# Kernel optimization log

Hardware: AMD Instinct MI355X
Metric: run time of the kernel (lower is better)

## Reference

```python
import jax, jax.numpy as jnp
import numpy as np

NUM_EXPERTS = 8
TOP_K = 2
HIDDEN = 1024
INTER = 3584
TOKENS = 16384


def setup_inputs() -> dict:
    key = jax.random.key(0)
    k0, k1, k2, k3, k4 = jax.random.split(key, 5)
    s = 0.02
    return {
        "hidden_states": jax.random.normal(k0, (TOKENS, HIDDEN), dtype=jnp.float32),
        "gate_w": jax.random.normal(k1, (NUM_EXPERTS, HIDDEN), dtype=jnp.float32) * s,
        "w1": jax.random.normal(k2, (NUM_EXPERTS, INTER, HIDDEN), dtype=jnp.float32) * s,
        "w3": jax.random.normal(k3, (NUM_EXPERTS, INTER, HIDDEN), dtype=jnp.float32) * s,
        "w2": jax.random.normal(k4, (NUM_EXPERTS, HIDDEN, INTER), dtype=jnp.float32) * s,
    }


def reference(hidden_states, gate_w, w1, w3, w2):
    # Router: logits -> softmax -> top-k -> renormalize (Mixtral gating)
    router_logits = jnp.einsum("th,eh->te", hidden_states, gate_w)  # [T, E]
    probs = jax.nn.softmax(router_logits, axis=-1)
    topk_w, topk_idx = jax.lax.top_k(probs, TOP_K)                  # [T, K]
    topk_w = topk_w / jnp.sum(topk_w, axis=-1, keepdims=True)
    # Dense combine weights: [T, E], zero for unselected experts
    combine = jnp.sum(
        jax.nn.one_hot(topk_idx, NUM_EXPERTS, dtype=hidden_states.dtype)
        * topk_w[..., None],
        axis=1,
    )
    out = jnp.zeros_like(hidden_states)
    for e in range(NUM_EXPERTS):  # small fixed expert loop
        h = jnp.einsum("th,ih->ti", hidden_states, w1[e])   # gate proj
        u = jnp.einsum("th,ih->ti", hidden_states, w3[e])   # up proj
        act = jax.nn.silu(h) * u                             # SwiGLU
        y = jnp.einsum("ti,hi->th", act, w2[e])              # down proj
        out = out + combine[:, e:e + 1] * y
    return out
```

## Files before the change

### kernel.cpp

```cpp
#include <hip/hip_runtime.h>
#include <hip/hip_bf16.h>

#define T_TOKENS 16384
#define HID 1024
#define NEXP 8
#define INTER 3584
#define PAIRS (2*T_TOKENS)
#define PAD_MAX (PAIRS + NEXP*128)

using f32x4    = __attribute__((ext_vector_type(4))) float;
using bfrag    = __attribute__((ext_vector_type(8))) short;
using float4_t = __attribute__((ext_vector_type(4))) float;
using ushort8_t = __attribute__((ext_vector_type(8))) unsigned short;

__device__ inline unsigned short f2bf(float f){
    unsigned u = __float_as_uint(f);
    u += 0x7FFFu + ((u >> 16) & 1u);
    return (unsigned short)(u >> 16);
}

__device__ inline void gload16(const unsigned short* g, unsigned short* l){
    __builtin_amdgcn_global_load_lds(
        (const __attribute__((address_space(1))) void*)g,
        (__attribute__((address_space(3))) void*)l, 16, 0, 0);
}

#define BAR_VM8() asm volatile("s_waitcnt vmcnt(8)\n\ts_barrier" ::: "memory")
#define BAR_VM0() asm volatile("s_waitcnt vmcnt(0)\n\ts_barrier" ::: "memory")
#define BAR_PLAIN() asm volatile("s_barrier" ::: "memory")

__device__ inline int xcd_swz(int flat, int nwg){
    int q = nwg >> 3, r = nwg & 7;
    int xcd = flat & 7, idx = flat >> 3;
    return (xcd < r ? xcd*(q+1) : r*(q+1) + (xcd - r)*q) + idx;
}

__device__ inline void st_decode(int sw, int nM, int nP, int STM,
                                 int& mt, int& p){
    int stSize = STM * nP;
    int st = sw / stSize;
    int rem = sw - st * stSize;
    int base = st * STM;
    int stM = (base + STM <= nM) ? STM : (nM - base);
    p  = rem / stM;
    mt = base + (rem - p * stM);
}

__global__ __launch_bounds__(256) void conv_bf16_kernel(
    const float* __restrict__ in, unsigned short* __restrict__ out, int n)
{
    int i0 = (blockIdx.x * 256 + threadIdx.x) * 8;
    int stride = gridDim.x * 256 * 8;
    for (int i = i0; i < n; i += stride){
        float4_t a = *reinterpret_cast<const float4_t*>(in + i);
        float4_t b = *reinterpret_cast<const float4_t*>(in + i + 4);
        ushort8_t o;
        o[0]=f2bf(a.x); o[1]=f2bf(a.y); o[2]=f2bf(a.z); o[3]=f2bf(a.w);
        o[4]=f2bf(b.x); o[5]=f2bf(b.y); o[6]=f2bf(b.z); o[7]=f2bf(b.w);
        *reinterpret_cast<ushort8_t*>(out + i) = o;
    }
}

__global__ __launch_bounds__(256) void router_kernel(
    const float* __restrict__ x, const float* __restrict__ gw,
    int* __restrict__ topk_idx, float* __restrict__ topk_w)
{
    int wave = threadIdx.x >> 6;
    int lane = threadIdx.x & 63;
    int t = blockIdx.x * 4 + wave;

    float acc[NEXP];
#pragma unroll
    for (int e = 0; e < NEXP; ++e) acc[e] = 0.f;

    const float* xr = x + (size_t)t * HID;
    for (int hb = 0; hb < HID; hb += 64){
        float xv = xr[hb + lane];
#pragma unroll
        for (int e = 0; e < NEXP; ++e)
            acc[e] += xv * gw[e * HID + hb + lane];
    }
#pragma unroll
    for (int e = 0; e < NEXP; ++e){
#pragma unroll
        for (int s = 32; s > 0; s >>= 1)
            acc[e] += __shfl_xor(acc[e], s, 64);
    }
    if (lane == 0){
        int e0 = 0; float m0 = acc[0];
#pragma unroll
        for (int e = 1; e < NEXP; ++e) if (acc[e] > m0){ m0 = acc[e]; e0 = e; }
        int e1 = -1; float m1 = -1e30f;
#pragma unroll
        for (int e = 0; e < NEXP; ++e) if (e != e0 && acc[e] > m1){ m1 = acc[e]; e1 = e; }
        float p1 = __expf(m1 - m0);
        float inv = 1.f / (1.f + p1);
        topk_idx[2*t]   = e0;
        topk_idx[2*t+1] = e1;
        topk_w[2*t]   = inv;
        topk_w[2*t+1] = p1 * inv;
    }
}

__global__ __launch_bounds__(256) void hist_kernel(
    const int* __restrict__ topk_idx, int* __restrict__ counts)
{
    __shared__ int h[NEXP];
    if (threadIdx.x < NEXP) h[threadIdx.x] = 0;
    __syncthreads();
    int i0 = blockIdx.x * 256 + threadIdx.x;
    for (int i = i0; i < PAIRS; i += gridDim.x * 256)
        atomicAdd(&h[topk_idx[i]], 1);
    __syncthreads();
    if (threadIdx.x < NEXP) atomicAdd(&counts[threadIdx.x], h[threadIdx.x]);
}

__global__ void scan_kernel(const int* __restrict__ counts, int* __restrict__ offp)
{
    if (threadIdx.x == 0 && blockIdx.x == 0){
        int s = 0;
        for (int e = 0; e < NEXP; ++e){
            offp[e] = s;
            s += (counts[e] + 127) & ~127;
        }
        offp[NEXP] = s;
    }
}

__global__ __launch_bounds__(128) void padfill_kernel(
    const int* __restrict__ counts, const int* __restrict__ offp,
    int* __restrict__ pair_token, float* __restrict__ pair_w)
{
    int e = blockIdx.x;
    int base = offp[e];
    int aligned = offp[e+1] - base;
    for (int s = counts[e] + threadIdx.x; s < aligned; s += 128){
        pair_token[base + s] = (base + s) & (T_TOKENS - 1);
        pair_w[base + s] = 0.f;
    }
}

__global__ __launch_bounds__(256) void scatter_kernel(
    const int* __restrict__ topk_idx, const float* __restrict__ topk_w,
    const int* __restrict__ offp, int* __restrict__ cursors,
    int* __restrict__ pair_token, float* __restrict__ pair_w)
{
    __shared__ int hist[NEXP], base[NEXP], lcur[NEXP];
    int tid = threadIdx.x;
    if (tid < NEXP){ hist[tid] = 0; lcur[tid] = 0; }
    __syncthreads();

    int t = blockIdx.x * 256 + tid;
    int e0 = topk_idx[2*t], e1 = topk_idx[2*t + 1];
    atomicAdd(&hist[e0], 1);
    atomicAdd(&hist[e1], 1);
    __syncthreads();

    if (tid < NEXP) base[tid] = atomicAdd(&cursors[tid], hist[tid]);
    __syncthreads();

    int r0 = atomicAdd(&lcur[e0], 1);
    int r1 = atomicAdd(&lcur[e1], 1);
    int p0 = offp[e0] + base[e0] + r0;
    int p1 = offp[e1] + base[e1] + r1;
    pair_token[p0] = t;  pair_w[p0] = topk_w[2*t];
    pair_token[p1] = t;  pair_w[p1] = topk_w[2*t + 1];
}

__global__ __launch_bounds__(256) void gemm_act_kernel(
    const unsigned short* __restrict__ xb,
    const unsigned short* __restrict__ w1b,
    const unsigned short* __restrict__ w3b,
    const int* __restrict__ offp,
    const int* __restrict__ pair_token, const float* __restrict__ pair_w,
    unsigned short* __restrict__ act, int r0)
{
    int nP = gridDim.x, nM = gridDim.y;
    int sw = xcd_swz(blockIdx.y * nP + blockIdx.x, nP * nM);
    int mt, p;
    st_decode(sw, nM, nP, 8, mt, p);
    int by = mt, bx = p;

    int R = r0 + by * 128;
    if (R >= offp[NEXP]) return;
    int e = 0;
    while (offp[e+1] <= R) ++e;
    int icol0 = bx * 64;

    __shared__ alignas(16) unsigned short As0[128*64], As1[128*64];
    __shared__ alignas(16) unsigned short B10[64*64],  B11[64*64];
    __shared__ alignas(16) unsigned short B30[64*64],  B31[64*64];
    __shared__ int   toks[128];
    __shared__ float pws[128];

    int tid = threadIdx.x;
    if (tid < 128){
        toks[tid] = pair_token[R + tid];
        pws[tid]  = pair_w[R + tid];
    }
    __syncthreads();

    int w = tid >> 6, lane = tid & 63;
    int wm = w >> 1, wn = w & 1;
    int lr = lane >> 3;
    int l15 = lane & 15;
    int swz8 = ((lane & 7) ^ lr) * 8;

    size_t asrc[4];
#pragma unroll
    for (int i = 0; i < 4; ++i)
        asrc[i] = (size_t)toks[w*32 + i*8 + lr] * HID + swz8;

    const unsigned short* w1e = w1b + (size_t)e * INTER * HID;
    const unsigned short* w3e = w3b + (size_t)e * INTER * HID;
    size_t bsrc[2];
#pragma unroll
    for (int i = 0; i < 2; ++i)
        bsrc[i] = (size_t)(icol0 + w*16 + i*8 + lr) * HID + swz8;

    int ccol[2];
#pragma unroll
    for (int kk = 0; kk < 2; ++kk)
        ccol[kk] = (((kk*4 + (lane >> 4)) ^ (lane & 7)) * 8);

    f32x4 acc_h[4][2], acc_u[4][2];
#pragma unroll
    for (int m = 0; m < 4; ++m)
#pragma unroll
        for (int n = 0; n < 2; ++n){
            acc_h[m][n] = (f32x4){0.f,0.f,0.f,0.f};
            acc_u[m][n] = (f32x4){0.f,0.f,0.f,0.f};
        }

    auto stageT = [&](unsigned short* As, unsigned short* B1s, unsigned short* B3s, int t){
        int k0 = t * 64;
#pragma unroll
        for (int i = 0; i < 4; ++i) gload16(xb  + asrc[i] + k0, As  + (w*32 + i*8)*64);
#pragma unroll
        for (int i = 0; i < 2; ++i) gload16(w1e + bsrc[i] + k0, B1s + (w*16 + i*8)*64);
#pragma unroll
        for (int i = 0; i < 2; ++i) gload16(w3e + bsrc[i] + k0, B3s + (w*16 + i*8)*64);
    };

    auto computeT = [&](const unsigned short* As, const unsigned short* B1s, const unsigned short* B3s){
        __builtin_amdgcn_s_setprio(1);
#pragma unroll
        for (int kk = 0; kk < 2; ++kk){
            int cc = ccol[kk];
            bfrag a[4];
#pragma unroll
            for (int m = 0; m < 4; ++m)
                a[m] = *reinterpret_cast<const bfrag*>(&As[(wm*64 + m*16 + l15)*64 + cc]);
#pragma unroll
            for (int n = 0; n < 2; ++n){
                bfrag b1 = *reinterpret_cast<const bfrag*>(&B1s[(wn*32 + n*16 + l15)*64 + cc]);
                bfrag b3 = *reinterpret_cast<const bfrag*>(&B3s[(wn*32 + n*16 + l15)*64 + cc]);
#pragma unroll
                for (int m = 0; m < 4; ++m){
                    acc_h[m][n] = __builtin_amdgcn_mfma_f32_16x16x32_bf16(a[m], b1, acc_h[m][n], 0, 0, 0);
                    acc_u[m][n] = __builtin_amdgcn_mfma_f32_16x16x32_bf16(a[m], b3, acc_u[m][n], 0, 0, 0);
                }
            }
        }
        __builtin_amdgcn_s_setprio(0);
    };

    const int NT = HID / 64;
    stageT(As0, B10, B30, 0);
    stageT(As1, B11, B31, 1);
#pragma unroll 1
    for (int t = 0; t < NT - 2; t += 2){
        BAR_VM8();
        computeT(As0, B10, B30);
        BAR_PLAIN();
        stageT(As0, B10, B30, t + 2);
        BAR_VM8();
        computeT(As1, B11, B31);
        BAR_PLAIN();
        stageT(As1, B11, B31, t + 3);
    }
    BAR_VM8();
    computeT(As0, B10, B30);
    BAR_VM0();
    computeT(As1, B11, B31);

    size_t arow0 = (size_t)(by * 128) * INTER;
#pragma unroll
    for (int m = 0; m < 4; ++m){
#pragma unroll
        for (int n = 0; n < 2; ++n){
#pragma unroll
            for (int j = 0; j < 4; ++j){
                int rl = wm*64 + m*16 + (lane >> 4)*4 + j;
                float h = acc_h[m][n][j];
                float u = acc_u[m][n][j];
                float v = pws[rl] * h * u / (1.f + __expf(-h));
                int ic = icol0 + wn*32 + n*16 + l15;
                act[arow0 + (size_t)rl * INTER + ic] = f2bf(v);
            }
        }
    }
}

__global__ __launch_bounds__(256) void gemm2_kernel(
    const unsigned short* __restrict__ act,
    const unsigned short* __restrict__ w2b,
    const int* __restrict__ offp,
    const int* __restrict__ pair_token,
    float* __restrict__ out, int r0)
{
    int nP = gridDim.x, nM = gridDim.y;
    int sw = xcd_swz(blockIdx.y * nP + blockIdx.x, nP * nM);
    int mt, p;
    st_decode(sw, nM, nP, 4, mt, p);
    int by = mt, bx = p;

    int R = r0 + by * 128;
    if (R >= offp[NEXP]) return;
    int e = 0;
    while (offp[e+1] <= R) ++e;
    int h0 = bx * 128;

    __shared__ alignas(16) unsigned short As0[128*64], As1[128*64];
    __shared__ alignas(16) unsigned short Bs0[128*64], Bs1[128*64];
    __shared__ int toks[128];

    int tid = threadIdx.x;
    if (tid < 128) toks[tid] = pair_token[R + tid];
    __syncthreads();

    int w = tid >> 6, lane = tid & 63;
    int wm = w >> 1, wn = w & 1;
    int lr = lane >> 3;
    int l15 = lane & 15;
    int swz8 = ((lane & 7) ^ lr) * 8;

    const unsigned short* w2e = w2b + (size_t)e * HID * INTER;
    size_t arow0 = (size_t)(by * 128) * INTER;

    size_t asrc[4], bsrc[4];
#pragma unroll
    for (int i = 0; i < 4; ++i){
        asrc[i] = arow0 + (size_t)(w*32 + i*8 + lr) * INTER + swz8;
        bsrc[i] = (size_t)(h0 + w*32 + i*8 + lr) * INTER + swz8;
    }

    int ccol[2];
#pragma unroll
    for (int kk = 0; kk < 2; ++kk)
        ccol[kk] = (((kk*4 + (lane >> 4)) ^ (lane & 7)) * 8);

    f32x4 acc[4][4];
#pragma unroll
    for (int m = 0; m < 4; ++m)
#pragma unroll
        for (int n = 0; n < 4; ++n)
            acc[m][n] = (f32x4){0.f,0.f,0.f,0.f};

    auto stageT = [&](unsigned short* As, unsigned short* Bs, int t){
        int kc = t * 64;
#pragma unroll
        for (int i = 0; i < 4; ++i) gload16(act + asrc[i] + kc, As + (w*32 + i*8)*64);
#pragma unroll
        for (int i = 0; i < 4; ++i) gload16(w2e + bsrc[i] + kc, Bs + (w*32 + i*8)*64);
    };

    auto computeT = [&](const unsigned short* As, const unsigned short* Bs){
        __builtin_amdgcn_s_setprio(1);
#pragma unroll
        for (int kk = 0; kk < 2; ++kk){
            int cc = ccol[kk];
            bfrag a[4];
#pragma unroll
            for (int m = 0; m < 4; ++m)
                a[m] = *reinterpret_cast<const bfrag*>(&As[(wm*64 + m*16 + l15)*64 + cc]);
#pragma unroll
            for (int n = 0; n < 4; ++n){
                bfrag b = *reinterpret_cast<const bfrag*>(&Bs[(wn*64 + n*16 + l15)*64 + cc]);
#pragma unroll
                for (int m = 0; m < 4; ++m)
                    acc[m][n] = __builtin_amdgcn_mfma_f32_16x16x32_bf16(a[m], b, acc[m][n], 0, 0, 0);
            }
        }
        __builtin_amdgcn_s_setprio(0);
    };

    const int NT = INTER / 64;
    stageT(As0, Bs0, 0);
    stageT(As1, Bs1, 1);
#pragma unroll 1
    for (int t = 0; t < NT - 2; t += 2){
        BAR_VM8();
        computeT(As0, Bs0);
        BAR_PLAIN();
        stageT(As0, Bs0, t + 2);
        BAR_VM8();
        computeT(As1, Bs1);
        BAR_PLAIN();
        stageT(As1, Bs1, t + 3);
    }
    BAR_VM8();
    computeT(As0, Bs0);
    BAR_VM0();
    computeT(As1, Bs1);

#pragma unroll
    for (int m = 0; m < 4; ++m){
#pragma unroll
        for (int n = 0; n < 4; ++n){
#pragma unroll
            for (int j = 0; j < 4; ++j){
                int rl = wm*64 + m*16 + (lane >> 4)*4 + j;
                int hc = h0 + wn*64 + n*16 + l15;
                atomicAdd(&out[(size_t)toks[rl] * HID + hc], acc[m][n][j]);
            }
        }
    }
}

extern "C" void kernel_launch(void* const* d_in, const int* in_sizes, int n_in,
                              void* d_out, int out_size, void* d_ws, size_t ws_size,
                              hipStream_t stream)
{
    const float* x  = (const float*)d_in[0];
    const float* gw = (const float*)d_in[1];
    const float* w1 = (const float*)d_in[2];
    const float* w3 = (const float*)d_in[3];
    const float* w2 = (const float*)d_in[4];
    float* out = (float*)d_out;

    char* ws = (char*)d_ws;
    size_t off = 0;
    auto bump = [&](size_t bytes) -> void* {
        void* p = ws + off;
        off = (off + bytes + 255) & ~(size_t)255;
        return p;
    };
    int*   counts     = (int*)bump(32);
    int*   cursors    = (int*)bump(32);
    int*   offp       = (int*)bump(64);
    int*   topk_idx   = (int*)bump((size_t)PAIRS * 4);
    float* topk_w     = (float*)bump((size_t)PAIRS * 4);
    int*   pair_token = (int*)bump((size_t)PAD_MAX * 4);
    float* pair_w     = (float*)bump((size_t)PAD_MAX * 4);
    unsigned short* xb  = (unsigned short*)bump((size_t)T_TOKENS * HID * 2);
    unsigned short* w1b = (unsigned short*)bump((size_t)NEXP * INTER * HID * 2);
    unsigned short* w3b = (unsigned short*)bump((size_t)NEXP * INTER * HID * 2);
    unsigned short* w2b = (unsigned short*)bump((size_t)NEXP * HID * INTER * 2);
    unsigned short* act = (unsigned short*)(ws + off);

    size_t rem = (ws_size > off) ? (ws_size - off) : 0;
    int RC = (int)(rem / ((size_t)INTER * 2));
    RC &= ~127;
    if (RC > PAD_MAX) RC = PAD_MAX;
    if (RC < 128) RC = 128;
    int nchunks = (PAD_MAX + RC - 1) / RC;

    hipMemsetAsync(d_out, 0, (size_t)T_TOKENS * HID * 4, stream);
    hipMemsetAsync(ws, 0, 1024, stream);

    conv_bf16_kernel<<<2048, 256, 0, stream>>>(x,  xb,  T_TOKENS * HID);
    conv_bf16_kernel<<<2048, 256, 0, stream>>>(w1, w1b, NEXP * INTER * HID);
    conv_bf16_kernel<<<2048, 256, 0, stream>>>(w3, w3b, NEXP * INTER * HID);
    conv_bf16_kernel<<<2048, 256, 0, stream>>>(w2, w2b, NEXP * HID * INTER);

    router_kernel<<<T_TOKENS/4, 256, 0, stream>>>(x, gw, topk_idx, topk_w);
    hist_kernel<<<64, 256, 0, stream>>>(topk_idx, counts);
    scan_kernel<<<1, 64, 0, stream>>>(counts, offp);
    padfill_kernel<<<NEXP, 128, 0, stream>>>(counts, offp, pair_token, pair_w);
    scatter_kernel<<<T_TOKENS/256, 256, 0, stream>>>(topk_idx, topk_w, offp, cursors,
                                                     pair_token, pair_w);

    for (int c = 0; c < nchunks; ++c){
        int r0 = c * RC;
        gemm_act_kernel<<<dim3(INTER/64, RC/128), 256, 0, stream>>>(
            xb, w1b, w3b, offp, pair_token, pair_w, act, r0);
        gemm2_kernel<<<dim3(HID/128, RC/128), 256, 0, stream>>>(
            act, w2b, offp, pair_token, out, r0);
    }
}
```

Measured before the change: 1.069 ms.

## Split GEMM K-loop into half-tile phases with finer vmcnt waits, fuse conversions

Both expert GEMM kernels now split each K-tile into two phases. A-fragments are held in registers and each phase computes half the N columns. Global-to-LDS loads for the next tile are issued between the LDS reads and the MFMAs, guarded by partial vmcnt waits rather than a full barrier-plus-prefetch pattern. Separately, the three weight conversions are merged into one launch and the activation bf16 conversion is folded into the router kernel. This aims to cut barrier stalls and launch overhead, at the cost of more registers and tighter dependence on exact vmcnt counts.

New measurement: 1.931 ms. 1.81x slower.

```diff
diff --git a/kernel.cpp b/kernel.cpp
--- a/kernel.cpp
+++ b/kernel.cpp
@@ -25,9 +25,9 @@
         (__attribute__((address_space(3))) void*)l, 16, 0, 0);
 }
 
-#define BAR_VM8() asm volatile("s_waitcnt vmcnt(8)\n\ts_barrier" ::: "memory")
+#define BAR_VM2() asm volatile("s_waitcnt vmcnt(2)\n\ts_barrier" ::: "memory")
+#define BAR_VM4() asm volatile("s_waitcnt vmcnt(4)\n\ts_barrier" ::: "memory")
 #define BAR_VM0() asm volatile("s_waitcnt vmcnt(0)\n\ts_barrier" ::: "memory")
-#define BAR_PLAIN() asm volatile("s_barrier" ::: "memory")
 
 __device__ inline int xcd_swz(int flat, int nwg){
     int q = nwg >> 3, r = nwg & 7;
@@ -46,9 +46,15 @@
     mt = base + (rem - p * stM);
 }
 
-__global__ __launch_bounds__(256) void conv_bf16_kernel(
-    const float* __restrict__ in, unsigned short* __restrict__ out, int n)
-{
+__global__ __launch_bounds__(256) void conv3_kernel(
+    const float* __restrict__ w1, const float* __restrict__ w3,
+    const float* __restrict__ w2,
+    unsigned short* __restrict__ w1b, unsigned short* __restrict__ w3b,
+    unsigned short* __restrict__ w2b)
+{
+    const int n = NEXP * INTER * HID;
+    const float* in = (blockIdx.y == 0) ? w1 : (blockIdx.y == 1) ? w3 : w2;
+    unsigned short* out = (blockIdx.y == 0) ? w1b : (blockIdx.y == 1) ? w3b : w2b;
     int i0 = (blockIdx.x * 256 + threadIdx.x) * 8;
     int stride = gridDim.x * 256 * 8;
     for (int i = i0; i < n; i += stride){
@@ -63,7 +69,8 @@
 
 __global__ __launch_bounds__(256) void router_kernel(
     const float* __restrict__ x, const float* __restrict__ gw,
-    int* __restrict__ topk_idx, float* __restrict__ topk_w)
+    int* __restrict__ topk_idx, float* __restrict__ topk_w,
+    unsigned short* __restrict__ xb)
 {
     int wave = threadIdx.x >> 6;
     int lane = threadIdx.x & 63;
@@ -80,6 +87,19 @@
         for (int e = 0; e < NEXP; ++e)
             acc[e] += xv * gw[e * HID + hb + lane];
     }
+
+    unsigned short* xbr = xb + (size_t)t * HID;
+#pragma unroll
+    for (int r = 0; r < 2; ++r){
+        int c = (lane + r*64) * 8;
+        float4_t va = *reinterpret_cast<const float4_t*>(xr + c);
+        float4_t vb = *reinterpret_cast<const float4_t*>(xr + c + 4);
+        ushort8_t o;
+        o[0]=f2bf(va.x); o[1]=f2bf(va.y); o[2]=f2bf(va.z); o[3]=f2bf(va.w);
+        o[4]=f2bf(vb.x); o[5]=f2bf(vb.y); o[6]=f2bf(vb.z); o[7]=f2bf(vb.w);
+        *reinterpret_cast<ushort8_t*>(xbr + c) = o;
+    }
+
 #pragma unroll
     for (int e = 0; e < NEXP; ++e){
 #pragma unroll
@@ -213,10 +233,10 @@
 
     const unsigned short* w1e = w1b + (size_t)e * INTER * HID;
     const unsigned short* w3e = w3b + (size_t)e * INTER * HID;
-    size_t bsrc[2];
-#pragma unroll
-    for (int i = 0; i < 2; ++i)
-        bsrc[i] = (size_t)(icol0 + w*16 + i*8 + lr) * HID + swz8;
+
+    int gf = ((w & 2) * 2 + (w & 1)) * 8;
+    size_t bsrcF = (size_t)(icol0 + gf + lr) * HID + swz8;
+    size_t bsrcS = (size_t)(icol0 + gf + 16 + lr) * HID + swz8;
 
     int ccol[2];
 #pragma unroll
@@ -232,57 +252,101 @@
             acc_u[m][n] = (f32x4){0.f,0.f,0.f,0.f};
         }
 
-    auto stageT = [&](unsigned short* As, unsigned short* B1s, unsigned short* B3s, int t){
+    bfrag aF[4][2];
+
+    auto stageA = [&](unsigned short* Ad, int t){
         int k0 = t * 64;
 #pragma unroll
-        for (int i = 0; i < 4; ++i) gload16(xb  + asrc[i] + k0, As  + (w*32 + i*8)*64);
-#pragma unroll
-        for (int i = 0; i < 2; ++i) gload16(w1e + bsrc[i] + k0, B1s + (w*16 + i*8)*64);
-#pragma unroll
-        for (int i = 0; i < 2; ++i) gload16(w3e + bsrc[i] + k0, B3s + (w*16 + i*8)*64);
-    };
-
-    auto computeT = [&](const unsigned short* As, const unsigned short* B1s, const unsigned short* B3s){
+        for (int i = 0; i < 4; ++i) gload16(xb + asrc[i] + k0, Ad + (w*32 + i*8)*64);
+    };
+    auto stageBfirst = [&](unsigned short* B1d, unsigned short* B3d, int t){
+        int k0 = t * 64;
+        gload16(w1e + bsrcF + k0, B1d + gf*64);
+        gload16(w3e + bsrcF + k0, B3d + gf*64);
+    };
+    auto stageBsecond = [&](unsigned short* B1d, unsigned short* B3d, int t){
+        int k0 = t * 64;
+        gload16(w1e + bsrcS + k0, B1d + (gf+16)*64);
+        gload16(w3e + bsrcS + k0, B3d + (gf+16)*64);
+    };
+
+    auto phase0 = [&](const unsigned short* As, const unsigned short* B1s,
+                      const unsigned short* B3s, unsigned short* Ad,
+                      bool issue, int tn){
+#pragma unroll
+        for (int m = 0; m < 4; ++m)
+#pragma unroll
+            for (int kk = 0; kk < 2; ++kk)
+                aF[m][kk] = *reinterpret_cast<const bfrag*>(
+                    &As[(wm*64 + m*16 + l15)*64 + ccol[kk]]);
+        bfrag b1[2], b3[2];
+#pragma unroll
+        for (int kk = 0; kk < 2; ++kk){
+            b1[kk] = *reinterpret_cast<const bfrag*>(&B1s[(wn*32 + l15)*64 + ccol[kk]]);
+            b3[kk] = *reinterpret_cast<const bfrag*>(&B3s[(wn*32 + l15)*64 + ccol[kk]]);
+        }
+        if (issue) stageA(Ad, tn);
         __builtin_amdgcn_s_setprio(1);
 #pragma unroll
+        for (int kk = 0; kk < 2; ++kk)
+#pragma unroll
+            for (int m = 0; m < 4; ++m){
+                acc_h[m][0] = __builtin_amdgcn_mfma_f32_16x16x32_bf16(aF[m][kk], b1[kk], acc_h[m][0], 0, 0, 0);
+                acc_u[m][0] = __builtin_amdgcn_mfma_f32_16x16x32_bf16(aF[m][kk], b3[kk], acc_u[m][0], 0, 0, 0);
+            }
+        __builtin_amdgcn_s_setprio(0);
+    };
+
+    auto phase1 = [&](const unsigned short* B1s, const unsigned short* B3s,
+                      unsigned short* B1d, unsigned short* B3d,
+                      bool issue, int tn){
+        bfrag b1[2], b3[2];
+#pragma unroll
         for (int kk = 0; kk < 2; ++kk){
-            int cc = ccol[kk];
-            bfrag a[4];
-#pragma unroll
-            for (int m = 0; m < 4; ++m)
-                a[m] = *reinterpret_cast<const bfrag*>(&As[(wm*64 + m*16 + l15)*64 + cc]);
-#pragma unroll
-            for (int n = 0; n < 2; ++n){
-                bfrag b1 = *reinterpret_cast<const bfrag*>(&B1s[(wn*32 + n*16 + l15)*64 + cc]);
-                bfrag b3 = *reinterpret_cast<const bfrag*>(&B3s[(wn*32 + n*16 + l15)*64 + cc]);
-#pragma unroll
-                for (int m = 0; m < 4; ++m){
-                    acc_h[m][n] = __builtin_amdgcn_mfma_f32_16x16x32_bf16(a[m], b1, acc_h[m][n], 0, 0, 0);
-                    acc_u[m][n] = __builtin_amdgcn_mfma_f32_16x16x32_bf16(a[m], b3, acc_u[m][n], 0, 0, 0);
-                }
+            b1[kk] = *reinterpret_cast<const bfrag*>(&B1s[(wn*32 + 16 + l15)*64 + ccol[kk]]);
+            b3[kk] = *reinterpret_cast<const bfrag*>(&B3s[(wn*32 + 16 + l15)*64 + ccol[kk]]);
+        }
+        if (issue){
+            stageBfirst(B1d, B3d, tn);
+            __builtin_amdgcn_sched_barrier(0);
+            stageBsecond(B1d, B3d, tn);
+        }
+        __builtin_amdgcn_s_setprio(1);
+#pragma unroll
+        for (int kk = 0; kk < 2; ++kk)
+#pragma unroll
+            for (int m = 0; m < 4; ++m){
+                acc_h[m][1] = __builtin_amdgcn_mfma_f32_16x16x32_bf16(aF[m][kk], b1[kk], acc_h[m][1], 0, 0, 0);
+                acc_u[m][1] = __builtin_amdgcn_mfma_f32_16x16x32_bf16(aF[m][kk], b3[kk], acc_u[m][1], 0, 0, 0);
             }
-        }
         __builtin_amdgcn_s_setprio(0);
     };
 
     const int NT = HID / 64;
-    stageT(As0, B10, B30, 0);
-    stageT(As1, B11, B31, 1);
+    stageA(As0, 0);
+    stageBfirst(B10, B30, 0);
+    __builtin_amdgcn_sched_barrier(0);
+    stageBsecond(B10, B30, 0);
+
 #pragma unroll 1
     for (int t = 0; t < NT - 2; t += 2){
-        BAR_VM8();
-        computeT(As0, B10, B30);
-        BAR_PLAIN();
-        stageT(As0, B10, B30, t + 2);
-        BAR_VM8();
-        computeT(As1, B11, B31);
-        BAR_PLAIN();
-        stageT(As1, B11, B31, t + 3);
-    }
-    BAR_VM8();
-    computeT(As0, B10, B30);
+        BAR_VM2();
+        phase0(As0, B10, B30, As1, true, t+1);
+        BAR_VM4();
+        phase1(B10, B30, B11, B31, true, t+1);
+        BAR_VM2();
+        phase0(As1, B11, B31, As0, true, t+2);
+        BAR_VM4();
+        phase1(B11, B31, B10, B30, true, t+2);
+    }
+    BAR_VM2();
+    phase0(As0, B10, B30, As1, true, NT-1);
+    BAR_VM4();
+    phase1(B10, B30, B11, B31, true, NT-1);
+    BAR_VM2();
+    phase0(As1, B11, B31, nullptr, false, 0);
     BAR_VM0();
-    computeT(As1, B11, B31);
+    phase1(B11, B31, nullptr, nullptr, false, 0);
 
     size_t arow0 = (size_t)(by * 128) * INTER;
 #pragma unroll
@@ -338,12 +402,16 @@
     const unsigned short* w2e = w2b + (size_t)e * HID * INTER;
     size_t arow0 = (size_t)(by * 128) * INTER;
 
-    size_t asrc[4], bsrc[4];
-#pragma unroll
-    for (int i = 0; i < 4; ++i){
+    size_t asrc[4];
+#pragma unroll
+    for (int i = 0; i < 4; ++i)
         asrc[i] = arow0 + (size_t)(w*32 + i*8 + lr) * INTER + swz8;
-        bsrc[i] = (size_t)(h0 + w*32 + i*8 + lr) * INTER + swz8;
-    }
+
+    int gr0 = w*8, gr1 = 64 + w*8, gr2 = 32 + w*8, gr3 = 96 + w*8;
+    size_t bsrc0 = (size_t)(h0 + gr0 + lr) * INTER + swz8;
+    size_t bsrc1 = (size_t)(h0 + gr1 + lr) * INTER + swz8;
+    size_t bsrc2 = (size_t)(h0 + gr2 + lr) * INTER + swz8;
+    size_t bsrc3 = (size_t)(h0 + gr3 + lr) * INTER + swz8;
 
     int ccol[2];
 #pragma unroll
@@ -357,52 +425,101 @@
         for (int n = 0; n < 4; ++n)
             acc[m][n] = (f32x4){0.f,0.f,0.f,0.f};
 
-    auto stageT = [&](unsigned short* As, unsigned short* Bs, int t){
+    bfrag aF[4][2];
+
+    auto stageA = [&](unsigned short* Ad, int t){
         int kc = t * 64;
 #pragma unroll
-        for (int i = 0; i < 4; ++i) gload16(act + asrc[i] + kc, As + (w*32 + i*8)*64);
-#pragma unroll
-        for (int i = 0; i < 4; ++i) gload16(w2e + bsrc[i] + kc, Bs + (w*32 + i*8)*64);
-    };
-
-    auto computeT = [&](const unsigned short* As, const unsigned short* Bs){
+        for (int i = 0; i < 4; ++i) gload16(act + asrc[i] + kc, Ad + (w*32 + i*8)*64);
+    };
+    auto stageBfirst = [&](unsigned short* Bd, int t){
+        int kc = t * 64;
+        gload16(w2e + bsrc0 + kc, Bd + gr0*64);
+        gload16(w2e + bsrc1 + kc, Bd + gr1*64);
+    };
+    auto stageBsecond = [&](unsigned short* Bd, int t){
+        int kc = t * 64;
+        gload16(w2e + bsrc2 + kc, Bd + gr2*64);
+        gload16(w2e + bsrc3 + kc, Bd + gr3*64);
+    };
+
+    auto phase0 = [&](const unsigned short* As, const unsigned short* Bs,
+                      unsigned short* Ad, bool issue, int tn){
+#pragma unroll
+        for (int m = 0; m < 4; ++m)
+#pragma unroll
+            for (int kk = 0; kk < 2; ++kk)
+                aF[m][kk] = *reinterpret_cast<const bfrag*>(
+                    &As[(wm*64 + m*16 + l15)*64 + ccol[kk]]);
+        bfrag b[2][2];
+#pragma unroll
+        for (int n = 0; n < 2; ++n)
+#pragma unroll
+            for (int kk = 0; kk < 2; ++kk)
+                b[n][kk] = *reinterpret_cast<const bfrag*>(
+                    &Bs[(wn*64 + n*16 + l15)*64 + ccol[kk]]);
+        if (issue) stageA(Ad, tn);
         __builtin_amdgcn_s_setprio(1);
 #pragma unroll
-        for (int kk = 0; kk < 2; ++kk){
-            int cc = ccol[kk];
-            bfrag a[4];
-#pragma unroll
-            for (int m = 0; m < 4; ++m)
-                a[m] = *reinterpret_cast<const bfrag*>(&As[(wm*64 + m*16 + l15)*64 + cc]);
-#pragma unroll
-            for (int n = 0; n < 4; ++n){
-                bfrag b = *reinterpret_cast<const bfrag*>(&Bs[(wn*64 + n*16 + l15)*64 + cc]);
+        for (int kk = 0; kk < 2; ++kk)
+#pragma unroll
+            for (int n = 0; n < 2; ++n)
 #pragma unroll
                 for (int m = 0; m < 4; ++m)
-                    acc[m][n] = __builtin_amdgcn_mfma_f32_16x16x32_bf16(a[m], b, acc[m][n], 0, 0, 0);
-            }
-        }
+                    acc[m][n] = __builtin_amdgcn_mfma_f32_16x16x32_bf16(aF[m][kk], b[n][kk], acc[m][n], 0, 0, 0);
         __builtin_amdgcn_s_setprio(0);
     };
 
+    auto phase1 = [&](const unsigned short* Bs, unsigned short* Bd,
+                      bool issue, int tn){
+        bfrag b[2][2];
+#pragma unroll
+        for (int n = 0; n < 2; ++n)
+#pragma unroll
+            for (int kk = 0; kk < 2; ++kk)
+                b[n][kk] = *reinterpret_cast<const bfrag*>(
+                    &Bs[(wn*64 + (n+2)*16 + l15)*64 + ccol[kk]]);
+        if (issue){
+            stageBfirst(Bd, tn);
+            __builtin_amdgcn_sched_barrier(0);
+            stageBsecond(Bd, tn);
+        }
+        __builtin_amdgcn_s_setprio(1);
+#pragma unroll
+        for (int kk = 0; kk < 2; ++kk)
+#pragma unroll
+            for (int n = 0; n < 2; ++n)
+#pragma unroll
+                for (int m = 0; m < 4; ++m)
+                    acc[m][n+2] = __builtin_amdgcn_mfma_f32_16x16x32_bf16(aF[m][kk], b[n][kk], acc[m][n+2], 0, 0, 0);
+        __builtin_amdgcn_s_setprio(0);
+    };
+
     const int NT = INTER / 64;
-    stageT(As0, Bs0, 0);
-    stageT(As1, Bs1, 1);
+    stageA(As0, 0);
+    stageBfirst(Bs0, 0);
+    __builtin_amdgcn_sched_barrier(0);
+    stageBsecond(Bs0, 0);
+
 #pragma unroll 1
     for (int t = 0; t < NT - 2; t += 2){
-        BAR_VM8();
-        computeT(As0, Bs0);
-        BAR_PLAIN();
-        stageT(As0, Bs0, t + 2);
-        BAR_VM8();
-        computeT(As1, Bs1);
-        BAR_PLAIN();
-        stageT(As1, Bs1, t + 3);
-    }
-    BAR_VM8();
-    computeT(As0, Bs0);
+        BAR_VM2();
+        phase0(As0, Bs0, As1, true, t+1);
+        BAR_VM4();
+        phase1(Bs0, Bs1, true, t+1);
+        BAR_VM2();
+        phase0(As1, Bs1, As0, true, t+2);
+        BAR_VM4();
+        phase1(Bs1, Bs0, true, t+2);
+    }
+    BAR_VM2();
+    phase0(As0, Bs0, As1, true, NT-1);
+    BAR_VM4();
+    phase1(Bs0, Bs1, true, NT-1);
+    BAR_VM2();
+    phase0(As1, Bs1, nullptr, false, 0);
     BAR_VM0();
-    computeT(As1, Bs1);
+    phase1(Bs1, nullptr, false, 0);
 
 #pragma unroll
     for (int m = 0; m < 4; ++m){
@@ -459,12 +576,9 @@
     hipMemsetAsync(d_out, 0, (size_t)T_TOKENS * HID * 4, stream);
     hipMemsetAsync(ws, 0, 1024, stream);
 
-    conv_bf16_kernel<<<2048, 256, 0, stream>>>(x,  xb,  T_TOKENS * HID);
-    conv_bf16_kernel<<<2048, 256, 0, stream>>>(w1, w1b, NEXP * INTER * HID);
-    conv_bf16_kernel<<<2048, 256, 0, stream>>>(w3, w3b, NEXP * INTER * HID);
-    conv_bf16_kernel<<<2048, 256, 0, stream>>>(w2, w2b, NEXP * HID * INTER);
-
-    router_kernel<<<T_TOKENS/4, 256, 0, stream>>>(x, gw, topk_idx, topk_w);
+    conv3_kernel<<<dim3(768, 3), 256, 0, stream>>>(w1, w3, w2, w1b, w3b, w2b);
+
+    router_kernel<<<T_TOKENS/4, 256, 0, stream>>>(x, gw, topk_idx, topk_w, xb);
     hist_kernel<<<64, 256, 0, stream>>>(topk_idx, counts);
     scan_kernel<<<1, 64, 0, stream>>>(counts, offp);
     padfill_kernel<<<NEXP, 128, 0, stream>>>(counts, offp, pair_token, pair_w);
```
